# Kernel tuning notes

Measured on AMD Instinct MI355X. Metric: run time of the kernel, lower is better.

## Reference

```python
import jax, jax.numpy as jnp
import numpy as np

LAM = 0.1   # smooth_param
EPS = 1e-8  # torch cosine_similarity eps


def setup_inputs() -> dict:
    key = jax.random.key(0)
    k1, k2, k3 = jax.random.split(key, 3)
    B, num_supp, num_query, T, D = 8, 5, 128, 16, 2048
    supp = jax.random.normal(k1, (B, num_supp, T, D), jnp.float32)
    query = jax.random.normal(k2, (B, num_query, T, D), jnp.float32)
    query_ys = jax.random.randint(k3, (B * num_query,), 0, num_supp)
    return {"supp": supp, "query": query, "query_ys": query_ys}


def _cosine_dist(supp, query):
    # supp: (B, ns, T, D), query: (B, nq, T, D)
    # dist[b,q,s,l,m] = 1 - cos(supp[b,s,l], query[b,q,m]); batch order (b,q,s)
    B, ns, T, D = supp.shape
    nq = query.shape[1]
    dots = jnp.einsum('bsld,bqmd->bqslm', supp, query)
    sn = jnp.linalg.norm(supp, axis=-1)   # (B, ns, T)
    qn = jnp.linalg.norm(query, axis=-1)  # (B, nq, T)
    denom = jnp.maximum(sn[:, None, :, :, None] * qn[:, :, None, None, :], EPS)
    dist = 1.0 - dots / denom
    return dist.reshape(B * nq * ns, T, T)


def _dtw(dist):
    # Relaxed (soft-min) OTAM band DP. dist: (N, T, T) -> (N,)
    # opt grid is (T, T+2) with zero-padded columns m=0 and m=T+1.
    N, T, _ = dist.shape
    dist_pad = jnp.pad(dist, ((0, 0), (0, 0), (1, 1)))  # (N, T, T+2)
    # Row l=0: opt[0,m] = cumsum of dist_pad[0, :m+1]
    row0 = jnp.cumsum(dist_pad[:, 0, :], axis=-1)  # (N, T+2)

    m_idx = jnp.arange(1, T + 2)
    boundary = (m_idx == 1) | (m_idx == T + 1)  # 3-way softmin only at band edges

    def row_step(prev_row, dist_row):
        # prev_row: (N, T+2) = opt[l-1]; dist_row: (N, T+2) = dist_pad[:, l]
        def col_step(left, xs):
            diag, up, d, is_b = xs  # each (N,) except is_b scalar bool
            s2 = jnp.logaddexp(-diag / LAM, -left / LAM)        # {diag, left}
            s3 = jnp.logaddexp(s2, -up / LAM)                   # + {up}
            val = -LAM * jnp.where(is_b, s3, s2) + d
            return val, val

        xs = (prev_row[:, :-1].T, prev_row[:, 1:].T, dist_row[:, 1:].T, boundary)
        init = jnp.zeros((N,), dist_row.dtype)  # opt[l, 0] = 0
        _, cols = jax.lax.scan(col_step, init, xs)  # (T+1, N)
        new_row = jnp.concatenate([init[:, None], cols.T], axis=1)  # (N, T+2)
        return new_row, None

    rows = jnp.swapaxes(dist_pad[:, 1:, :], 0, 1)  # (T-1, N, T+2)
    final_row, _ = jax.lax.scan(row_step, row0, rows)
    return final_row[:, -1]  # opt[:, T-1, T+1]


def _cross_entropy(logits, labels):
    logp = jax.nn.log_softmax(logits, axis=-1)
    return -jnp.mean(jnp.take_along_axis(logp, labels[:, None], axis=1))


def reference(supp, query, query_ys):
    ns = supp.shape[1]
    dist = _cosine_dist(supp, query)            # (B*nq*ns, T, T)
    tam1 = _dtw(dist).reshape(-1, ns)           # forward-direction alignment
    tam2 = _dtw(dist[:, ::-1, ::-1]).reshape(-1, ns)  # flipped (dims 1,2)
    loss1 = _cross_entropy(-tam1, query_ys)
    loss2 = _cross_entropy(-tam2, query_ys)
    loss = 0.5 * (loss1 + loss2)
    tam = 0.5 * (tam1 + tam2)
    return loss, tam
```

## Files before the change

kernel.cpp:

```cpp
#include <hip/hip_runtime.h>
#include <hip/hip_bf16.h>

#define NB   8
#define NS   5
#define TT   16
#define DD   2048
#define NROW 1024
#define NSROW 640
#define TILESH (TT * DD)
#define LDS_ROW 2056
#define LAMI 10.0f
#define LAMF 0.1f

typedef __attribute__((ext_vector_type(8))) short  short8;
typedef __attribute__((ext_vector_type(4))) float  float4v;

static __device__ __forceinline__ unsigned int cvtpk(float x, float y) {
    unsigned int r;
    asm("v_cvt_pk_bf16_f32 %0, %1, %2" : "=v"(r) : "v"(x), "v"(y));
    return r;
}

static __device__ __forceinline__ float dpp_shr1(float x) {
    int r = __builtin_amdgcn_update_dpp(0, __builtin_bit_cast(int, x),
                                        0x138 , 0xF, 0xF, true);
    return __builtin_bit_cast(float, r);
}

static __device__ __forceinline__ void
dtw_and_out(const float (*distS)[TT][TT], float* tamv, int tid, int blk,
            const int* __restrict__ ys, float* __restrict__ out)
{
    const int wave = tid >> 6, lane = tid & 63;
    {
        const int grp  = lane / 21;
        const int g    = lane - grp * 21;
        const int slot = wave * 3 + grp;
        float val = 0.f, vprev = 0.f;
        if (grp < 3 && slot < 10 && g <= 17) {
            const int s    = slot >> 1;
            const int dir  = slot & 1;
            const bool isb = (g == 1) | (g == 17);
            #pragma unroll
            for (int t = 1; t <= 32; ++t) {
                float left = dpp_shr1(val);
                float diag = dpp_shr1(vprev);
                int l = t - g;
                if (g >= 1 && l >= 0 && l <= 15) {
                    float d = 0.f;
                    if (g <= 16) d = dir ? distS[s][15 - l][16 - g] : distS[s][l][g - 1];
                    float nv;
                    if (l == 0) {
                        nv = left + d;
                    } else {
                        float am = -LAMI * diag, bm = -LAMI * left;
                        float mx = fmaxf(am, bm);
                        float s3 = 0.f;
                        if (isb) {
                            float cm = -LAMI * val;
                            float m3 = fmaxf(mx, cm);
                            s3 = __expf(cm - m3);
                            mx = m3;
                        }
                        float ssum = __expf(am - mx) + __expf(bm - mx) + s3;
                        nv = fmaf(-LAMF, mx + __logf(ssum), d);
                    }
                    vprev = val; val = nv;
                }
            }
            if (g == 17) tamv[slot] = val;
        }
    }
    __syncthreads();

    if (tid < NS) out[1 + blk * NS + tid] = 0.5f * (tamv[2 * tid] + tamv[2 * tid + 1]);
    if (tid == 0) {
        float t1v[NS], t2v[NS];
        #pragma unroll
        for (int s = 0; s < NS; ++s) { t1v[s] = tamv[2 * s]; t2v[s] = tamv[2 * s + 1]; }
        const int y = ys[blk];
        float mx1 = -t1v[0], mx2 = -t2v[0];
        #pragma unroll
        for (int s = 1; s < NS; ++s) { mx1 = fmaxf(mx1, -t1v[s]); mx2 = fmaxf(mx2, -t2v[s]); }
        float s1 = 0.f, s2 = 0.f;
        #pragma unroll
        for (int s = 0; s < NS; ++s) { s1 += __expf(-t1v[s] - mx1); s2 += __expf(-t2v[s] - mx2); }
        float lse1  = mx1 + __logf(s1);
        float lse2v = mx2 + __logf(s2);
        float ty1 = t1v[0], ty2 = t2v[0];
        #pragma unroll
        for (int s = 1; s < NS; ++s) { if (y == s) { ty1 = t1v[s]; ty2 = t2v[s]; } }
        float c = 0.5f * ((lse1 + ty1) + (lse2v + ty2));
        atomicAdd(out, c * (1.0f / (float)NROW));
    }
}

__global__ __launch_bounds__(256) void
pack_supp(const float* __restrict__ supp, unsigned short* __restrict__ sPk,
          float* __restrict__ loss0)
{
    if (blockIdx.x == 0 && threadIdx.x == 0) loss0[0] = 0.f;
    const int wave = threadIdx.x >> 6, lane = threadIdx.x & 63;
    const int row = blockIdx.x * 4 + wave;
    const float* src = supp + (size_t)row * DD;
    unsigned short* dstTile = sPk + (size_t)(row >> 4) * TILESH;
    const int fr = row & 15;

    float4 v[4][2];
    float ss = 0.f;
    #pragma unroll
    for (int it = 0; it < 4; ++it) {
        v[it][0] = *reinterpret_cast<const float4*>(src + it * 512 + lane * 8);
        v[it][1] = *reinterpret_cast<const float4*>(src + it * 512 + lane * 8 + 4);
        #pragma unroll
        for (int h = 0; h < 2; ++h)
            ss += v[it][h].x * v[it][h].x + v[it][h].y * v[it][h].y
                + v[it][h].z * v[it][h].z + v[it][h].w * v[it][h].w;
    }
    #pragma unroll
    for (int off = 32; off >= 1; off >>= 1) ss += __shfl_xor(ss, off, 64);
    const float rs = 1.0f / sqrtf(fmaxf(ss, 1e-16f));

    #pragma unroll
    for (int it = 0; it < 4; ++it) {
        uint4 pv;
        pv.x = cvtpk(v[it][0].x * rs, v[it][0].y * rs);
        pv.y = cvtpk(v[it][0].z * rs, v[it][0].w * rs);
        pv.z = cvtpk(v[it][1].x * rs, v[it][1].y * rs);
        pv.w = cvtpk(v[it][1].z * rs, v[it][1].w * rs);
        const int kk = it * 16 + (lane >> 2);
        const int c  = lane & 3;
        *reinterpret_cast<uint4*>(dstTile + kk * 512 + (c * 16 + fr) * 8) = pv;
    }
}

__global__ __launch_bounds__(256, 2) void
dist_dtw_fused(const unsigned short* __restrict__ sPk, const float* __restrict__ query,
               const int* __restrict__ ys, float* __restrict__ out)
{
    __shared__ __align__(16) unsigned char smem[TT * LDS_ROW * 2];
    unsigned short (*sB)[LDS_ROW] = reinterpret_cast<unsigned short(*)[LDS_ROW]>(smem);
    float (*red)[NS][64][4] = reinterpret_cast<float(*)[NS][64][4]>(smem);
    float (*distS)[TT][TT]  = reinterpret_cast<float(*)[TT][TT]>(smem + 20480);
    float* tamv             = reinterpret_cast<float*>(smem + 25600);

    const int tid  = threadIdx.x;
    const int blk  = blockIdx.x;
    const int wave = tid >> 6;
    const int lane = tid & 63;
    const int fr   = lane & 15;
    const int quad = lane >> 4;

    #pragma unroll
    for (int j = 0; j < 4; ++j) {
        const int r = wave * 4 + j;
        const float* src = query + (size_t)(blk * TT + r) * DD;
        float4 v[8];
        float ss = 0.f;
        #pragma unroll
        for (int i = 0; i < 8; ++i) {
            v[i] = *reinterpret_cast<const float4*>(src + i * 256 + lane * 4);
            ss += v[i].x * v[i].x + v[i].y * v[i].y + v[i].z * v[i].z + v[i].w * v[i].w;
        }
        #pragma unroll
        for (int off = 32; off >= 1; off >>= 1) ss += __shfl_xor(ss, off, 64);
        const float rs = 1.0f / sqrtf(fmaxf(ss, 1e-16f));
        #pragma unroll
        for (int i = 0; i < 8; ++i) {
            uint2 pv = { cvtpk(v[i].x * rs, v[i].y * rs), cvtpk(v[i].z * rs, v[i].w * rs) };
            *reinterpret_cast<uint2*>(&sB[r][i * 256 + lane * 4]) = pv;
        }
    }
    __syncthreads();

    float4v acc[NS];
    #pragma unroll
    for (int s = 0; s < NS; ++s) acc[s] = (float4v){0.f, 0.f, 0.f, 0.f};

    const unsigned short* sp = sPk + (size_t)(blk >> 7) * NS * TILESH
                             + (size_t)(wave * 16) * 512 + lane * 8;
    const unsigned short* bb = &sB[fr][(wave * 16) * 32 + quad * 8];

    #pragma unroll 2
    for (int kk = 0; kk < 16; ++kk) {
        short8 b = *reinterpret_cast<const short8*>(bb + kk * 32);
        #pragma unroll
        for (int s = 0; s < NS; ++s) {
            short8 a = *reinterpret_cast<const short8*>(sp + (size_t)s * TILESH + kk * 512);
            acc[s] = __builtin_amdgcn_mfma_f32_16x16x32_bf16(a, b, acc[s], 0, 0, 0);
        }
    }
    __syncthreads();

    #pragma unroll
    for (int s = 0; s < NS; ++s)
        *reinterpret_cast<float4v*>(red[wave][s][lane]) = acc[s];
    __syncthreads();

    for (int p = tid; p < NS * 64; p += 256) {
        int t = p >> 6, ln = p & 63;
        float4v s4 = *reinterpret_cast<const float4v*>(red[0][t][ln]);
        #pragma unroll
        for (int w = 1; w < 4; ++w) {
            float4v r = *reinterpret_cast<const float4v*>(red[w][t][ln]);
            s4[0] += r[0]; s4[1] += r[1]; s4[2] += r[2]; s4[3] += r[3];
        }
        int m = ln & 15, qd = ln >> 4;
        #pragma unroll
        for (int r = 0; r < 4; ++r) distS[t][qd * 4 + r][m] = 1.0f - s4[r];
    }
    __syncthreads();

    dtw_and_out(distS, tamv, tid, blk, ys, out);
}

extern "C" void kernel_launch(void* const* d_in, const int* in_sizes, int n_in,
                              void* d_out, int out_size, void* d_ws, size_t ws_size,
                              hipStream_t stream) {
    const float* supp  = (const float*)d_in[0];
    const float* query = (const float*)d_in[1];
    const int*   ys    = (const int*)d_in[2];
    float* out = (float*)d_out;

    unsigned short* sPk = (unsigned short*)d_ws;

    pack_supp<<<NSROW / 4, 256, 0, stream>>>(supp, sPk, out);
    dist_dtw_fused<<<NROW, 256, 0, stream>>>(sPk, query, ys, out);
}
```

Baseline: 225.3 us.

## Stage query in two K-halves with deferred normalization to raise occupancy

```diff
diff --git a/kernel.cpp b/kernel.cpp
--- a/kernel.cpp
+++ b/kernel.cpp
@@ -8,7 +8,7 @@
 #define NROW 1024
 #define NSROW 640
 #define TILESH (TT * DD)
-#define LDS_ROW 2056
+#define LDH  1032
 #define LAMI 10.0f
 #define LAMF 0.1f
 
@@ -134,15 +134,16 @@
     }
 }
 
-__global__ __launch_bounds__(256, 2) void
-dist_dtw_fused(const unsigned short* __restrict__ sPk, const float* __restrict__ query,
-               const int* __restrict__ ys, float* __restrict__ out)
+__global__ __launch_bounds__(256, 4) void
+dist_dtw_f2(const unsigned short* __restrict__ sPk, const float* __restrict__ query,
+            const int* __restrict__ ys, float* __restrict__ out)
 {
-    __shared__ __align__(16) unsigned char smem[TT * LDS_ROW * 2];
-    unsigned short (*sB)[LDS_ROW] = reinterpret_cast<unsigned short(*)[LDS_ROW]>(smem);
+    __shared__ __align__(16) unsigned char smem[TT * LDH * 2];
+    unsigned short (*sB)[LDH] = reinterpret_cast<unsigned short(*)[LDH]>(smem);
     float (*red)[NS][64][4] = reinterpret_cast<float(*)[NS][64][4]>(smem);
     float (*distS)[TT][TT]  = reinterpret_cast<float(*)[TT][TT]>(smem + 20480);
-    float* tamv             = reinterpret_cast<float*>(smem + 25600);
+    __shared__ float qq[16];
+    __shared__ float tamv[12];
 
     const int tid  = threadIdx.x;
     const int blk  = blockIdx.x;
@@ -151,50 +152,57 @@
     const int fr   = lane & 15;
     const int quad = lane >> 4;
 
-    #pragma unroll
-    for (int j = 0; j < 4; ++j) {
-        const int r = wave * 4 + j;
-        const float* src = query + (size_t)(blk * TT + r) * DD;
-        float4 v[8];
-        float ss = 0.f;
-        #pragma unroll
-        for (int i = 0; i < 8; ++i) {
-            v[i] = *reinterpret_cast<const float4*>(src + i * 256 + lane * 4);
-            ss += v[i].x * v[i].x + v[i].y * v[i].y + v[i].z * v[i].z + v[i].w * v[i].w;
-        }
-        #pragma unroll
-        for (int off = 32; off >= 1; off >>= 1) ss += __shfl_xor(ss, off, 64);
-        const float rs = 1.0f / sqrtf(fmaxf(ss, 1e-16f));
-        #pragma unroll
-        for (int i = 0; i < 8; ++i) {
-            uint2 pv = { cvtpk(v[i].x * rs, v[i].y * rs), cvtpk(v[i].z * rs, v[i].w * rs) };
-            *reinterpret_cast<uint2*>(&sB[r][i * 256 + lane * 4]) = pv;
-        }
-    }
-    __syncthreads();
-
     float4v acc[NS];
     #pragma unroll
     for (int s = 0; s < NS; ++s) acc[s] = (float4v){0.f, 0.f, 0.f, 0.f};
-
-    const unsigned short* sp = sPk + (size_t)(blk >> 7) * NS * TILESH
-                             + (size_t)(wave * 16) * 512 + lane * 8;
-    const unsigned short* bb = &sB[fr][(wave * 16) * 32 + quad * 8];
-
-    #pragma unroll 2
-    for (int kk = 0; kk < 16; ++kk) {
-        short8 b = *reinterpret_cast<const short8*>(bb + kk * 32);
-        #pragma unroll
-        for (int s = 0; s < NS; ++s) {
-            short8 a = *reinterpret_cast<const short8*>(sp + (size_t)s * TILESH + kk * 512);
-            acc[s] = __builtin_amdgcn_mfma_f32_16x16x32_bf16(a, b, acc[s], 0, 0, 0);
-        }
-    }
-    __syncthreads();
+    float qs[4] = {0.f, 0.f, 0.f, 0.f};
+
+    const unsigned short* spBase = sPk + (size_t)(blk >> 7) * NS * TILESH + lane * 8;
+
+    #pragma unroll
+    for (int h = 0; h < 2; ++h) {
+        #pragma unroll
+        for (int j = 0; j < 4; ++j) {
+            const int r = wave * 4 + j;
+            const float* src = query + (size_t)(blk * TT + r) * DD + h * 1024;
+            #pragma unroll
+            for (int i = 0; i < 2; ++i) {
+                float4 v0 = *reinterpret_cast<const float4*>(src + i * 512 + lane * 8);
+                float4 v1 = *reinterpret_cast<const float4*>(src + i * 512 + lane * 8 + 4);
+                uint4 pv = { cvtpk(v0.x, v0.y), cvtpk(v0.z, v0.w),
+                             cvtpk(v1.x, v1.y), cvtpk(v1.z, v1.w) };
+                *reinterpret_cast<uint4*>(&sB[r][i * 512 + lane * 8]) = pv;
+                qs[j] += v0.x*v0.x + v0.y*v0.y + v0.z*v0.z + v0.w*v0.w
+                       + v1.x*v1.x + v1.y*v1.y + v1.z*v1.z + v1.w*v1.w;
+            }
+        }
+        __syncthreads();
+
+        const unsigned short* bb = &sB[fr][wave * 256 + quad * 8];
+        #pragma unroll
+        for (int kk = 0; kk < 8; ++kk) {
+            short8 b = *reinterpret_cast<const short8*>(bb + kk * 32);
+            const int kkg = h * 32 + wave * 8 + kk;
+            #pragma unroll
+            for (int s = 0; s < NS; ++s) {
+                short8 a = *reinterpret_cast<const short8*>(
+                    spBase + (size_t)s * TILESH + (size_t)kkg * 512);
+                acc[s] = __builtin_amdgcn_mfma_f32_16x16x32_bf16(a, b, acc[s], 0, 0, 0);
+            }
+        }
+        __syncthreads();
+    }
 
     #pragma unroll
     for (int s = 0; s < NS; ++s)
         *reinterpret_cast<float4v*>(red[wave][s][lane]) = acc[s];
+    #pragma unroll
+    for (int j = 0; j < 4; ++j) {
+        float ss = qs[j];
+        #pragma unroll
+        for (int off = 32; off >= 1; off >>= 1) ss += __shfl_xor(ss, off, 64);
+        if (lane == 0) qq[wave * 4 + j] = ss;
+    }
     __syncthreads();
 
     for (int p = tid; p < NS * 64; p += 256) {
@@ -206,8 +214,9 @@
             s4[0] += r[0]; s4[1] += r[1]; s4[2] += r[2]; s4[3] += r[3];
         }
         int m = ln & 15, qd = ln >> 4;
-        #pragma unroll
-        for (int r = 0; r < 4; ++r) distS[t][qd * 4 + r][m] = 1.0f - s4[r];
+        float rq = 1.0f / sqrtf(fmaxf(qq[m], 1e-16f));
+        #pragma unroll
+        for (int r = 0; r < 4; ++r) distS[t][qd * 4 + r][m] = 1.0f - s4[r] * rq;
     }
     __syncthreads();
 
@@ -225,5 +234,5 @@
     unsigned short* sPk = (unsigned short*)d_ws;
 
     pack_supp<<<NSROW / 4, 256, 0, stream>>>(supp, sPk, out);
-    dist_dtw_fused<<<NROW, 256, 0, stream>>>(sPk, query, ys, out);
-}
+    dist_dtw_f2<<<NROW, 256, 0, stream>>>(sPk, query, ys, out);
+}
```

Result: slower. 239.9 us (+6.5%).

## Split fused kernel K-loop per support, 512 threads, two-phase query staging

Applied to the files above, without the earlier changes.

```diff
diff --git a/kernel.cpp b/kernel.cpp
--- a/kernel.cpp
+++ b/kernel.cpp
@@ -8,7 +8,7 @@
 #define NROW 1024
 #define NSROW 640
 #define TILESH (TT * DD)
-#define LDS_ROW 2056
+#define LDH  1032
 #define LAMI 10.0f
 #define LAMF 0.1f
 
@@ -28,48 +28,44 @@
 }
 
 static __device__ __forceinline__ void
-dtw_and_out(const float (*distS)[TT][TT], float* tamv, int tid, int blk,
+dtw_tail512(const float (*distS)[TT][TT], float* tamv, int tid, int blk,
             const int* __restrict__ ys, float* __restrict__ out)
 {
     const int wave = tid >> 6, lane = tid & 63;
-    {
-        const int grp  = lane / 21;
-        const int g    = lane - grp * 21;
-        const int slot = wave * 3 + grp;
+    if (wave < NS && (lane & 31) <= 17) {
+        const int g    = lane & 31;
+        const int dir  = lane >> 5;
+        const int s    = wave;
+        const bool isb = (g == 1) | (g == 17);
         float val = 0.f, vprev = 0.f;
-        if (grp < 3 && slot < 10 && g <= 17) {
-            const int s    = slot >> 1;
-            const int dir  = slot & 1;
-            const bool isb = (g == 1) | (g == 17);
-            #pragma unroll
-            for (int t = 1; t <= 32; ++t) {
-                float left = dpp_shr1(val);
-                float diag = dpp_shr1(vprev);
-                int l = t - g;
-                if (g >= 1 && l >= 0 && l <= 15) {
-                    float d = 0.f;
-                    if (g <= 16) d = dir ? distS[s][15 - l][16 - g] : distS[s][l][g - 1];
-                    float nv;
-                    if (l == 0) {
-                        nv = left + d;
-                    } else {
-                        float am = -LAMI * diag, bm = -LAMI * left;
-                        float mx = fmaxf(am, bm);
-                        float s3 = 0.f;
-                        if (isb) {
-                            float cm = -LAMI * val;
-                            float m3 = fmaxf(mx, cm);
-                            s3 = __expf(cm - m3);
-                            mx = m3;
-                        }
-                        float ssum = __expf(am - mx) + __expf(bm - mx) + s3;
-                        nv = fmaf(-LAMF, mx + __logf(ssum), d);
+        #pragma unroll
+        for (int t = 1; t <= 32; ++t) {
+            float left = dpp_shr1(val);
+            float diag = dpp_shr1(vprev);
+            int l = t - g;
+            if (g >= 1 && l >= 0 && l <= 15) {
+                float d = 0.f;
+                if (g <= 16) d = dir ? distS[s][15 - l][16 - g] : distS[s][l][g - 1];
+                float nv;
+                if (l == 0) {
+                    nv = left + d;
+                } else {
+                    float am = -LAMI * diag, bm = -LAMI * left;
+                    float mx = fmaxf(am, bm);
+                    float s3 = 0.f;
+                    if (isb) {
+                        float cm = -LAMI * val;
+                        float m3 = fmaxf(mx, cm);
+                        s3 = __expf(cm - m3);
+                        mx = m3;
                     }
-                    vprev = val; val = nv;
+                    float ssum = __expf(am - mx) + __expf(bm - mx) + s3;
+                    nv = fmaf(-LAMF, mx + __logf(ssum), d);
                 }
+                vprev = val; val = nv;
             }
-            if (g == 17) tamv[slot] = val;
-        }
+        }
+        if (g == 17) tamv[s * 2 + dir] = val;
     }
     __syncthreads();
 
@@ -134,15 +130,14 @@
     }
 }
 
-__global__ __launch_bounds__(256, 2) void
-dist_dtw_fused(const unsigned short* __restrict__ sPk, const float* __restrict__ query,
-               const int* __restrict__ ys, float* __restrict__ out)
+__global__ __launch_bounds__(512, 8) void
+dist_dtw_pk2(const unsigned short* __restrict__ sPk, const float* __restrict__ query,
+             const int* __restrict__ ys, float* __restrict__ out)
 {
-    __shared__ __align__(16) unsigned char smem[TT * LDS_ROW * 2];
-    unsigned short (*sB)[LDS_ROW] = reinterpret_cast<unsigned short(*)[LDS_ROW]>(smem);
-    float (*red)[NS][64][4] = reinterpret_cast<float(*)[NS][64][4]>(smem);
-    float (*distS)[TT][TT]  = reinterpret_cast<float(*)[TT][TT]>(smem + 20480);
-    float* tamv             = reinterpret_cast<float*>(smem + 25600);
+    __shared__ __align__(16) unsigned short sB[TT][LDH];
+    __shared__ float distS[NS][TT][TT];
+    __shared__ float qq[16];
+    __shared__ float tamv[12];
 
     const int tid  = threadIdx.x;
     const int blk  = blockIdx.x;
@@ -151,67 +146,58 @@
     const int fr   = lane & 15;
     const int quad = lane >> 4;
 
-    #pragma unroll
-    for (int j = 0; j < 4; ++j) {
-        const int r = wave * 4 + j;
-        const float* src = query + (size_t)(blk * TT + r) * DD;
-        float4 v[8];
-        float ss = 0.f;
-        #pragma unroll
-        for (int i = 0; i < 8; ++i) {
-            v[i] = *reinterpret_cast<const float4*>(src + i * 256 + lane * 4);
-            ss += v[i].x * v[i].x + v[i].y * v[i].y + v[i].z * v[i].z + v[i].w * v[i].w;
-        }
-        #pragma unroll
-        for (int off = 32; off >= 1; off >>= 1) ss += __shfl_xor(ss, off, 64);
-        const float rs = 1.0f / sqrtf(fmaxf(ss, 1e-16f));
-        #pragma unroll
-        for (int i = 0; i < 8; ++i) {
-            uint2 pv = { cvtpk(v[i].x * rs, v[i].y * rs), cvtpk(v[i].z * rs, v[i].w * rs) };
-            *reinterpret_cast<uint2*>(&sB[r][i * 256 + lane * 4]) = pv;
-        }
-    }
+    const int qr = tid >> 5;
+    const int qc = tid & 31;
+
+    float4v acc0 = {0.f, 0.f, 0.f, 0.f}, acc1 = {0.f, 0.f, 0.f, 0.f};
+    const unsigned short* sp =
+        sPk + ((size_t)(blk >> 7) * NS + wave) * TILESH + lane * 8;
+
+    #pragma unroll
+    for (int h = 0; h < 2; ++h) {
+        {
+            const float* qsrc = query + (size_t)(blk * TT + qr) * DD + h * 1024;
+            float ss = 0.f;
+            #pragma unroll
+            for (int i = 0; i < 8; ++i) {
+                float4 v = *reinterpret_cast<const float4*>(qsrc + (qc + i * 32) * 4);
+                uint2 pv = { cvtpk(v.x, v.y), cvtpk(v.z, v.w) };
+                *reinterpret_cast<uint2*>(&sB[qr][(qc + i * 32) * 4]) = pv;
+                ss += v.x * v.x + v.y * v.y + v.z * v.z + v.w * v.w;
+            }
+            #pragma unroll
+            for (int off = 16; off >= 1; off >>= 1) ss += __shfl_xor(ss, off, 32);
+            if (qc == 0) { if (h == 0) qq[qr] = ss; else qq[qr] += ss; }
+        }
+        __syncthreads();
+
+        if (wave < NS) {
+            const unsigned short* a  = sp + (size_t)(h * 32) * 512;
+            const unsigned short* bp = &sB[fr][quad * 8];
+            #pragma unroll 8
+            for (int k2 = 0; k2 < 32; k2 += 2) {
+                short8 a0 = *reinterpret_cast<const short8*>(a + (size_t)k2 * 512);
+                short8 a1 = *reinterpret_cast<const short8*>(a + (size_t)(k2 + 1) * 512);
+                short8 b0 = *reinterpret_cast<const short8*>(bp + k2 * 32);
+                short8 b1 = *reinterpret_cast<const short8*>(bp + k2 * 32 + 32);
+                acc0 = __builtin_amdgcn_mfma_f32_16x16x32_bf16(a0, b0, acc0, 0, 0, 0);
+                acc1 = __builtin_amdgcn_mfma_f32_16x16x32_bf16(a1, b1, acc1, 0, 0, 0);
+            }
+        }
+        if (h == 0) __syncthreads();
+    }
+
     __syncthreads();
-
-    float4v acc[NS];
-    #pragma unroll
-    for (int s = 0; s < NS; ++s) acc[s] = (float4v){0.f, 0.f, 0.f, 0.f};
-
-    const unsigned short* sp = sPk + (size_t)(blk >> 7) * NS * TILESH
-                             + (size_t)(wave * 16) * 512 + lane * 8;
-    const unsigned short* bb = &sB[fr][(wave * 16) * 32 + quad * 8];
-
-    #pragma unroll 2
-    for (int kk = 0; kk < 16; ++kk) {
-        short8 b = *reinterpret_cast<const short8*>(bb + kk * 32);
-        #pragma unroll
-        for (int s = 0; s < NS; ++s) {
-            short8 a = *reinterpret_cast<const short8*>(sp + (size_t)s * TILESH + kk * 512);
-            acc[s] = __builtin_amdgcn_mfma_f32_16x16x32_bf16(a, b, acc[s], 0, 0, 0);
-        }
-    }
-    __syncthreads();
-
-    #pragma unroll
-    for (int s = 0; s < NS; ++s)
-        *reinterpret_cast<float4v*>(red[wave][s][lane]) = acc[s];
-    __syncthreads();
-
-    for (int p = tid; p < NS * 64; p += 256) {
-        int t = p >> 6, ln = p & 63;
-        float4v s4 = *reinterpret_cast<const float4v*>(red[0][t][ln]);
-        #pragma unroll
-        for (int w = 1; w < 4; ++w) {
-            float4v r = *reinterpret_cast<const float4v*>(red[w][t][ln]);
-            s4[0] += r[0]; s4[1] += r[1]; s4[2] += r[2]; s4[3] += r[3];
-        }
-        int m = ln & 15, qd = ln >> 4;
-        #pragma unroll
-        for (int r = 0; r < 4; ++r) distS[t][qd * 4 + r][m] = 1.0f - s4[r];
-    }
-    __syncthreads();
-
-    dtw_and_out(distS, tamv, tid, blk, ys, out);
+    if (wave < NS) {
+        float rq = 1.0f / sqrtf(fmaxf(qq[fr], 1e-16f));
+        #pragma unroll
+        for (int r = 0; r < 4; ++r) {
+            int l = quad * 4 + r;
+            distS[wave][l][fr] = 1.0f - (acc0[r] + acc1[r]) * rq;
+        }
+    }
+
+    dtw_tail512(distS, tamv, tid, blk, ys, out);
 }
 
 extern "C" void kernel_launch(void* const* d_in, const int* in_sizes, int n_in,
@@ -225,5 +211,5 @@
     unsigned short* sPk = (unsigned short*)d_ws;
 
     pack_supp<<<NSROW / 4, 256, 0, stream>>>(supp, sPk, out);
-    dist_dtw_fused<<<NROW, 256, 0, stream>>>(sPk, query, ys, out);
-}
+    dist_dtw_pk2<<<NROW, 512, 0, stream>>>(sPk, query, ys, out);
+}
```

Result: faster. 218.6 us (-3.0%).
